# Performance work log

Measured on AMD Instinct MI355X. Metric: run time of the kernel, lower is better.

The kernel has to match this reference:

```python
import jax, jax.numpy as jnp
import numpy as np

E = 1024
H = 16
D = E // H
NUM_BUCKETS = 320
MAX_DISTANCE = 800


def _relative_positions_bucket(relative_positions):
    # relative_positions: int32 [T, S]
    num_buckets = NUM_BUCKETS // 2  # 160
    relative_buckets = (relative_positions > 0).astype(jnp.int32) * num_buckets
    rel = jnp.abs(relative_positions)
    max_exact = num_buckets // 2  # 80
    is_small = rel < max_exact
    rel_f = jnp.maximum(rel, 1).astype(jnp.float32)
    large = jnp.log(rel_f / max_exact) / np.log(MAX_DISTANCE / max_exact) * (num_buckets - max_exact)
    large = (max_exact + large).astype(jnp.int32)
    large = jnp.minimum(large, num_buckets - 1)
    relative_buckets = relative_buckets + jnp.where(is_small, rel, large)
    return relative_buckets


def setup_inputs() -> dict:
    key = jax.random.key(0)
    ks = jax.random.split(key, 12)
    B, T = 2, 2048
    s = 0.02
    return {
        "hidden_states": jax.random.normal(ks[0], (B, T, E), dtype=jnp.float32),
        "q_w": jax.random.normal(ks[1], (E, E), dtype=jnp.float32) * s,
        "q_b": jnp.zeros((E,), dtype=jnp.float32),
        "k_w": jax.random.normal(ks[2], (E, E), dtype=jnp.float32) * s,
        "k_b": jnp.zeros((E,), dtype=jnp.float32),
        "v_w": jax.random.normal(ks[3], (E, E), dtype=jnp.float32) * s,
        "v_b": jnp.zeros((E,), dtype=jnp.float32),
        "out_w": jax.random.normal(ks[4], (E, E), dtype=jnp.float32) * s,
        "out_b": jnp.zeros((E,), dtype=jnp.float32),
        "rel_embed": jax.random.normal(ks[5], (NUM_BUCKETS, H), dtype=jnp.float32) * s,
        "gru_const": jnp.ones((1, H, 1, 1), dtype=jnp.float32),
        "gru_w": jax.random.normal(ks[6], (8, D), dtype=jnp.float32) * s,
        "gru_b": jnp.zeros((8,), dtype=jnp.float32),
    }


def reference(hidden_states, q_w, q_b, k_w, k_b, v_w, v_b, out_w, out_b,
              rel_embed, gru_const, gru_w, gru_b):
    B, T, _ = hidden_states.shape
    scaling = D ** (-0.5)

    # --- relative position bias: [H, T, T] ---
    ctx = jnp.arange(T, dtype=jnp.int32)[:, None]
    mem = jnp.arange(T, dtype=jnp.int32)[None, :]
    buckets = _relative_positions_bucket(mem - ctx)          # [T, T]
    position_bias = rel_embed[buckets]                        # [T, T, H]
    position_bias = jnp.transpose(position_bias, (2, 0, 1))   # [H, T, T]

    # --- gate (gru_rel_pos): per (b, h, t) scalar ---
    gated = hidden_states.reshape(B, T, H, D).transpose(0, 2, 1, 3)  # [B,H,T,D]
    proj = jnp.einsum('bhtd,ed->bhte', gated, gru_w) + gru_b         # [B,H,T,8]
    proj = proj.reshape(B, H, T, 2, 4).sum(-1)                        # [B,H,T,2]
    gate = jax.nn.sigmoid(proj)
    gate_a = gate[..., 0:1]
    gate_b = gate[..., 1:2]
    gate_out = gate_a * (gate_b * gru_const - 1.0) + 2.0              # [B,H,T,1]
    gated_position_bias = gate_out * position_bias[None]              # [B,H,T,T]

    # --- attention (same math as F.multi_head_attention_forward eager path) ---
    q = (hidden_states @ q_w.T + q_b).reshape(B, T, H, D).transpose(0, 2, 1, 3) * scaling
    k = (hidden_states @ k_w.T + k_b).reshape(B, T, H, D).transpose(0, 2, 1, 3)
    v = (hidden_states @ v_w.T + v_b).reshape(B, T, H, D).transpose(0, 2, 1, 3)

    scores = jnp.einsum('bhtd,bhsd->bhts', q, k) + gated_position_bias
    attn = jax.nn.softmax(scores, axis=-1)
    ctx_out = jnp.einsum('bhts,bhsd->bhtd', attn, v)                  # [B,H,T,D]
    ctx_out = ctx_out.transpose(0, 2, 1, 3).reshape(B, T, E)
    return ctx_out @ out_w.T + out_b
```

## Files before the change

kernel.cpp:

```cpp
#include <hip/hip_runtime.h>
#include <hip/hip_bf16.h>
#include <math.h>

typedef __bf16 bf16;
typedef __bf16 bf16x4 __attribute__((ext_vector_type(4)));
typedef __bf16 bf16x8 __attribute__((ext_vector_type(8)));
typedef float  f32x4  __attribute__((ext_vector_type(4)));
typedef unsigned u32x2 __attribute__((ext_vector_type(2)));
typedef unsigned u32x4 __attribute__((ext_vector_type(4)));

#define T_SEQ 2048
#define E_DIM 1024
#define H_NUM 16
#define D_DIM 64
#define NDELTA 4095
#define LOG2E 1.4426950408889634f

__device__ __forceinline__ void gld16(const bf16* g, bf16* l) {
  __builtin_amdgcn_global_load_lds((__attribute__((address_space(1))) void*)(g),
                                   (__attribute__((address_space(3))) void*)(l), 16, 0, 0);
}

__device__ __forceinline__ void qswap(unsigned &a, unsigned &b) {
  u32x2 t  = __builtin_amdgcn_permlane32_swap(a, b, false, false);
  u32x2 t2 = __builtin_amdgcn_permlane16_swap(t[0], t[1], false, false);
  a = t2[0]; b = t2[1];
}

__global__ void cast_bf16_kernel(const float* __restrict__ src, bf16* __restrict__ dst, int n4) {
  int i = blockIdx.x * blockDim.x + threadIdx.x;
  if (i >= n4) return;
  const float4 v = reinterpret_cast<const float4*>(src)[i];
  bf16x4 o;
  o[0] = (bf16)v.x; o[1] = (bf16)v.y; o[2] = (bf16)v.z; o[3] = (bf16)v.w;
  reinterpret_cast<bf16x4*>(dst)[i] = o;
}

__global__ void cast_w_kernel(const float* __restrict__ q_w, const float* __restrict__ k_w,
                              const float* __restrict__ v_w, const float* __restrict__ o_w,
                              bf16* __restrict__ wcat, bf16* __restrict__ wob) {
  int i = blockIdx.x * 256 + threadIdx.x;
  int sel = blockIdx.y;
  const float* src = (sel == 0) ? q_w : (sel == 1) ? k_w : (sel == 2) ? v_w : o_w;
  bf16* dst = (sel < 3) ? (wcat + (size_t)sel * 1048576) : wob;
  const float4 v = reinterpret_cast<const float4*>(src)[i];
  bf16x4 o;
  o[0] = (bf16)v.x; o[1] = (bf16)v.y; o[2] = (bf16)v.z; o[3] = (bf16)v.w;
  reinterpret_cast<bf16x4*>(dst)[i] = o;
}

__global__ void pb_kernel(const float* __restrict__ rel_embed, float* __restrict__ pbt) {
  int dd = blockIdx.x * 64 + threadIdx.x;
  if (dd >= NDELTA) return;
  int delta = dd - (T_SEQ - 1);
  int bucket = (delta > 0) ? 160 : 0;
  int rel = abs(delta);
  int v;
  if (rel < 80) {
    v = rel;
  } else {
    float rf = (float)(rel < 1 ? 1 : rel);
    float lf = logf(rf / 80.0f) * (80.0f / 2.302585092994046f);
    int lg = 80 + (int)lf;
    v = lg < 159 ? lg : 159;
  }
  bucket += v;
#pragma unroll
  for (int h = 0; h < H_NUM; h++)
    pbt[h * NDELTA + dd] = rel_embed[bucket * H_NUM + h];
}

__global__ __launch_bounds__(256)
void gate_kernel(const float* __restrict__ hs, const float* __restrict__ gru_w,
                 const float* __restrict__ gru_b, const float* __restrict__ gconst,
                 float* __restrict__ gate)
{
  __shared__ float w[512];
  int tid = threadIdx.x;
  w[tid] = gru_w[tid];
  w[tid + 256] = gru_w[tid + 256];
  __syncthreads();
  int idx = blockIdx.x * 256 + tid;
  int h  = idx & 15;
  int bt = idx >> 4;
  const float* x = hs + (size_t)bt * E_DIM + h * D_DIM;
  float acc[8] = {0,0,0,0,0,0,0,0};
  for (int d = 0; d < 64; d += 4) {
    float4 xv = *(const float4*)&x[d];
#pragma unroll
    for (int e = 0; e < 8; e++) {
      acc[e] += xv.x * w[e*64+d] + xv.y * w[e*64+d+1]
              + xv.z * w[e*64+d+2] + xv.w * w[e*64+d+3];
    }
  }
  float p0 = acc[0]+acc[1]+acc[2]+acc[3] + gru_b[0]+gru_b[1]+gru_b[2]+gru_b[3];
  float p1 = acc[4]+acc[5]+acc[6]+acc[7] + gru_b[4]+gru_b[5]+gru_b[6]+gru_b[7];
  float ga = 1.0f / (1.0f + expf(-p0));
  float gb = 1.0f / (1.0f + expf(-p1));
  float g = (ga * (gb * gconst[h] - 1.0f) + 2.0f) * LOG2E;
  int bb = bt >> 11;
  int t  = bt & (T_SEQ - 1);
  gate[((size_t)(bb * H_NUM + h)) * T_SEQ + t] = g;
}

template<int MODE, int N_TOTAL>
__global__ __launch_bounds__(256)
void gemm2_kernel(const bf16* __restrict__ A, const bf16* __restrict__ W,
                  const float* __restrict__ b0, const float* __restrict__ b1,
                  const float* __restrict__ b2, float qalpha,
                  void* __restrict__ out0, void* __restrict__ out1, void* __restrict__ out2)
{
  __shared__ bf16 As[128 * 32];
  __shared__ bf16 Bs[128 * 32];
  const int tid  = threadIdx.x;
  const int lane = tid & 63;
  const int wave = tid >> 6;
  const int m0 = blockIdx.y * 128;
  const int n0 = blockIdx.x * 128;
  const int wm = (wave >> 1) * 64;
  const int wn = (wave & 1) * 64;
  const int qd = lane >> 4;
  const int lm = lane & 15;

  const int row4 = lane >> 2;
  const int col8 = (lane & 3) * 8;
  const bf16* gA0 = A + (size_t)(m0 + wave * 32 + row4) * 1024 + col8;
  const bf16* gA1 = gA0 + (size_t)16 * 1024;
  const bf16* gB0 = W + (size_t)(n0 + wave * 32 + row4) * 1024 + col8;
  const bf16* gB1 = gB0 + (size_t)16 * 1024;
  bf16* lA0 = As + (wave * 2 + 0) * 512;
  bf16* lA1 = As + (wave * 2 + 1) * 512;
  bf16* lB0 = Bs + (wave * 2 + 0) * 512;
  bf16* lB1 = Bs + (wave * 2 + 1) * 512;

  f32x4 acc[4][4] = {};

  for (int k0 = 0; k0 < 1024; k0 += 32) {
    gld16(gA0 + k0, lA0);
    gld16(gA1 + k0, lA1);
    gld16(gB0 + k0, lB0);
    gld16(gB1 + k0, lB1);
    __syncthreads();
    bf16x8 af[4], bfr[4];
#pragma unroll
    for (int i = 0; i < 4; i++) {
      af[i]  = *(const bf16x8*)&As[(wm + i * 16 + lm) * 32 + qd * 8];
      bfr[i] = *(const bf16x8*)&Bs[(wn + i * 16 + lm) * 32 + qd * 8];
    }
#pragma unroll
    for (int im = 0; im < 4; im++)
#pragma unroll
      for (int in = 0; in < 4; in++)
        acc[im][in] = __builtin_amdgcn_mfma_f32_16x16x32_bf16(af[im], bfr[in], acc[im][in], 0, 0, 0);
    __syncthreads();
  }

  const int seg = n0 >> 10;
  const float* bias = (MODE == 0) ? b0 : (seg == 0 ? b0 : (seg == 1 ? b1 : b2));
  const float alpha = (MODE == 1 && seg == 0) ? qalpha : 1.0f;

#pragma unroll
  for (int im = 0; im < 4; im++) {
#pragma unroll
    for (int in = 0; in < 4; in++) {
      const int n  = n0 + wn + in * 16 + lm;
      const int n1 = n & 1023;
      const float bv = bias[n1];
      const int mb = m0 + wm + im * 16 + qd * 4;
      if (MODE == 0) {
        float* o = (float*)out0;
#pragma unroll
        for (int r = 0; r < 4; r++)
          o[(size_t)(mb + r) * 1024 + n1] = acc[im][in][r] + bv;
      } else if (seg == 2) {
        const int bb = mb >> 11;
        const int t  = mb & 2047;
        bf16x4 pk;
#pragma unroll
        for (int r = 0; r < 4; r++) pk[r] = (bf16)(acc[im][in][r] + bv);
        *(bf16x4*)&((bf16*)out2)[((size_t)(bb * 1024 + n1)) * 2048 + t] = pk;
      } else {
        bf16* o = (bf16*)(seg == 0 ? out0 : out1);
#pragma unroll
        for (int r = 0; r < 4; r++)
          o[(size_t)(mb + r) * 1024 + n1] = (bf16)((acc[im][in][r] + bv) * alpha);
      }
    }
  }
}

#define LK 72
__global__ __launch_bounds__(256)
void attn3_kernel(const bf16* __restrict__ Qg, const bf16* __restrict__ Kg,
                  const bf16* __restrict__ Vtg, const float* __restrict__ gate,
                  const float* __restrict__ pbt, bf16* __restrict__ ctx)
{
  __shared__ bf16 Ks[2][64 * LK];
  __shared__ bf16 Vs[2][64 * LK];
  __shared__ float pbs[2176];

  const int t0 = blockIdx.x * 128;
  const int h  = blockIdx.y;
  const int b  = blockIdx.z;
  const int tid  = threadIdx.x;
  const int lane = tid & 63;
  const int wave = tid >> 6;
  const int qd = lane >> 4;
  const int lm = lane & 15;

  for (int i = tid; i < 2176; i += 256) {
    int idx = i - t0 + 1920;
    pbs[i] = (idx >= 0 && idx < NDELTA) ? pbt[h * NDELTA + idx] : 0.0f;
  }

  bf16x8 qf[2][2];
  float g[2];
#pragma unroll
  for (int nb = 0; nb < 2; nb++) {
    const int q = t0 + wave * 32 + nb * 16 + lm;
    const bf16* qrow = Qg + (size_t)(b * T_SEQ + q) * E_DIM + h * D_DIM;
    qf[nb][0] = *(const bf16x8*)(qrow + qd * 8);
    qf[nb][1] = *(const bf16x8*)(qrow + 32 + qd * 8);
    g[nb] = gate[((size_t)(b * H_NUM + h)) * T_SEQ + q];
  }

  const int srow = tid >> 2;
  const int scol = (tid & 3) * 16;
  const bf16* kgp = Kg  + ((size_t)(b * T_SEQ) + srow) * E_DIM + h * D_DIM + scol;
  const bf16* vgp = Vtg + ((size_t)(b * 1024) + h * D_DIM + srow) * T_SEQ + scol;

  {
    bf16x8 a0 = *(const bf16x8*)kgp;
    bf16x8 a1 = *(const bf16x8*)(kgp + 8);
    bf16x8 c0 = *(const bf16x8*)vgp;
    bf16x8 c1 = *(const bf16x8*)(vgp + 8);
    *(bf16x8*)&Ks[0][srow * LK + scol]     = a0;
    *(bf16x8*)&Ks[0][srow * LK + scol + 8] = a1;
    *(bf16x8*)&Vs[0][srow * LK + scol]     = c0;
    *(bf16x8*)&Vs[0][srow * LK + scol + 8] = c1;
  }
  __syncthreads();

  f32x4 o[4][2] = {};
  float li[2] = {0.0f, 0.0f};

  for (int it = 0; it < T_SEQ / 64; it++) {
    const int s0 = it * 64;
    const int buf = it & 1;
    const bool more = (it + 1 < T_SEQ / 64);
    bf16x8 nk0, nk1, nv0, nv1;
    if (more) {
      const bf16* kn = kgp + (size_t)(s0 + 64) * E_DIM;
      const bf16* vn = vgp + (s0 + 64);
      nk0 = *(const bf16x8*)kn; nk1 = *(const bf16x8*)(kn + 8);
      nv0 = *(const bf16x8*)vn; nv1 = *(const bf16x8*)(vn + 8);
    }

    bf16x8 kf[4][2];
#pragma unroll
    for (int mb = 0; mb < 4; mb++) {
      kf[mb][0] = *(const bf16x8*)&Ks[buf][(16 * mb + lm) * LK + qd * 8];
      kf[mb][1] = *(const bf16x8*)&Ks[buf][(16 * mb + lm) * LK + 32 + qd * 8];
    }

    bf16x8 pf[2][2];
#pragma unroll
    for (int nb = 0; nb < 2; nb++) {
      f32x4 sc[4];
#pragma unroll
      for (int mb = 0; mb < 4; mb++) {
        f32x4 t = {};
        t = __builtin_amdgcn_mfma_f32_16x16x32_bf16(kf[mb][0], qf[nb][0], t, 0, 0, 0);
        t = __builtin_amdgcn_mfma_f32_16x16x32_bf16(kf[mb][1], qf[nb][1], t, 0, 0, 0);
        sc[mb] = t;
      }
      const int ib = s0 + 4 * qd + 127 - (wave * 32 + nb * 16 + lm);
      float rs = 0.0f;
      unsigned wlo[4], whi[4];
#pragma unroll
      for (int mb = 0; mb < 4; mb++) {
        bf16x4 pk;
#pragma unroll
        for (int r = 0; r < 4; r++) {
          float p = __builtin_amdgcn_exp2f(sc[mb][r] + g[nb] * pbs[ib + 16 * mb + r]);
          rs += p;
          pk[r] = (bf16)p;
        }
        u32x2 pw = __builtin_bit_cast(u32x2, pk);
        wlo[mb] = pw[0]; whi[mb] = pw[1];
      }
      li[nb] += rs;
      unsigned a0 = wlo[0], b0v = wlo[1], a1 = whi[0], b1v = whi[1];
      qswap(a0, b0v);
      qswap(a1, b1v);
      u32x4 h0; h0[0] = a0; h0[1] = a1; h0[2] = b0v; h0[3] = b1v;
      pf[nb][0] = __builtin_bit_cast(bf16x8, h0);
      unsigned c0 = wlo[2], d0v = wlo[3], c1 = whi[2], d1v = whi[3];
      qswap(c0, d0v);
      qswap(c1, d1v);
      u32x4 h1; h1[0] = c0; h1[1] = c1; h1[2] = d0v; h1[3] = d1v;
      pf[nb][1] = __builtin_bit_cast(bf16x8, h1);
    }

#pragma unroll
    for (int db = 0; db < 4; db++) {
      bf16x8 vf0 = *(const bf16x8*)&Vs[buf][(16 * db + lm) * LK + qd * 8];
      bf16x8 vf1 = *(const bf16x8*)&Vs[buf][(16 * db + lm) * LK + 32 + qd * 8];
#pragma unroll
      for (int nb = 0; nb < 2; nb++) {
        o[db][nb] = __builtin_amdgcn_mfma_f32_16x16x32_bf16(vf0, pf[nb][0], o[db][nb], 0, 0, 0);
        o[db][nb] = __builtin_amdgcn_mfma_f32_16x16x32_bf16(vf1, pf[nb][1], o[db][nb], 0, 0, 0);
      }
    }
    if (more) {
      *(bf16x8*)&Ks[buf ^ 1][srow * LK + scol]     = nk0;
      *(bf16x8*)&Ks[buf ^ 1][srow * LK + scol + 8] = nk1;
      *(bf16x8*)&Vs[buf ^ 1][srow * LK + scol]     = nv0;
      *(bf16x8*)&Vs[buf ^ 1][srow * LK + scol + 8] = nv1;
    }
    __syncthreads();
  }

#pragma unroll
  for (int nb = 0; nb < 2; nb++) {
    li[nb] += __shfl_xor(li[nb], 16);
    li[nb] += __shfl_xor(li[nb], 32);
  }
#pragma unroll
  for (int nb = 0; nb < 2; nb++) {
    const float inv = 1.0f / li[nb];
    const int q = t0 + wave * 32 + nb * 16 + lm;
    bf16* obase = ctx + (size_t)(b * T_SEQ + q) * E_DIM + h * D_DIM + 4 * qd;
#pragma unroll
    for (int db = 0; db < 4; db++) {
      bf16x4 ov;
      ov[0] = (bf16)(o[db][nb][0] * inv); ov[1] = (bf16)(o[db][nb][1] * inv);
      ov[2] = (bf16)(o[db][nb][2] * inv); ov[3] = (bf16)(o[db][nb][3] * inv);
      *(bf16x4*)&obase[16 * db] = ov;
    }
  }
}

extern "C" void kernel_launch(void* const* d_in, const int* in_sizes, int n_in,
                              void* d_out, int out_size, void* d_ws, size_t ws_size,
                              hipStream_t stream)
{
  const float* hs     = (const float*)d_in[0];
  const float* q_w    = (const float*)d_in[1];
  const float* q_b    = (const float*)d_in[2];
  const float* k_w    = (const float*)d_in[3];
  const float* k_b    = (const float*)d_in[4];
  const float* v_w    = (const float*)d_in[5];
  const float* v_b    = (const float*)d_in[6];
  const float* out_w  = (const float*)d_in[7];
  const float* out_b  = (const float*)d_in[8];
  const float* rel    = (const float*)d_in[9];
  const float* gconst = (const float*)d_in[10];
  const float* gru_w  = (const float*)d_in[11];
  const float* gru_b  = (const float*)d_in[12];

  char* p = (char*)d_ws;
  bf16* hsb  = (bf16*)p; p += (size_t)4096 * 1024 * 2;
  bf16* wcat = (bf16*)p; p += (size_t)3072 * 1024 * 2;
  bf16* wob  = (bf16*)p; p += (size_t)1024 * 1024 * 2;
  bf16* Qb   = (bf16*)p; p += (size_t)4096 * 1024 * 2;
  bf16* Kb   = (bf16*)p; p += (size_t)4096 * 1024 * 2;
  bf16* Vtb  = (bf16*)p; p += (size_t)2048 * 2048 * 2;
  bf16* ctxb = (bf16*)p; p += (size_t)4096 * 1024 * 2;
  float* gatep = (float*)p; p += (size_t)2 * H_NUM * T_SEQ * 4;
  float* pbt   = (float*)p; p += (size_t)H_NUM * NDELTA * 4;

  cast_bf16_kernel<<<4096, 256, 0, stream>>>(hs, hsb, 1048576);
  cast_w_kernel<<<dim3(1024, 4), 256, 0, stream>>>(q_w, k_w, v_w, out_w, wcat, wob);
  pb_kernel<<<64, 64, 0, stream>>>(rel, pbt);
  gate_kernel<<<256, 256, 0, stream>>>(hs, gru_w, gru_b, gconst, gatep);

  const float qalpha = 0.125f * LOG2E;
  gemm2_kernel<1, 3072><<<dim3(24, 32), 256, 0, stream>>>(
      hsb, wcat, q_b, k_b, v_b, qalpha, Qb, Kb, Vtb);

  attn3_kernel<<<dim3(T_SEQ / 128, H_NUM, 2), 256, 0, stream>>>(Qb, Kb, Vtb, gatep, pbt, ctxb);

  gemm2_kernel<0, 1024><<<dim3(8, 32), 256, 0, stream>>>(
      ctxb, wob, out_b, nullptr, nullptr, 1.0f, d_out, nullptr, nullptr);
}
```

Baseline: 223.5 us.

## Load K/V tiles directly into LDS with XOR swizzle and MFMA priority hints

The attention kernel's K and V tile loads now go straight from global memory into LDS through global_load_lds. This replaces the register-staged loads and the LDS stores at the end of each iteration. The padded LDS layout is dropped in favour of an XOR-swizzled column layout to avoid bank conflicts. s_setprio is also raised around the MFMA sections. The intent is to cut VGPR pressure and instruction overhead in the loop, and to overlap the prefetch better. The risk is that the async LDS writes rely on the existing barrier for correctness.

```diff
diff --git a/kernel.cpp b/kernel.cpp
--- a/kernel.cpp
+++ b/kernel.cpp
@@ -189,14 +189,13 @@
   }
 }
 
-#define LK 72
 __global__ __launch_bounds__(256)
 void attn3_kernel(const bf16* __restrict__ Qg, const bf16* __restrict__ Kg,
                   const bf16* __restrict__ Vtg, const float* __restrict__ gate,
                   const float* __restrict__ pbt, bf16* __restrict__ ctx)
 {
-  __shared__ bf16 Ks[2][64 * LK];
-  __shared__ bf16 Vs[2][64 * LK];
+  __shared__ bf16 Ks[2][64 * 64];
+  __shared__ bf16 Vs[2][64 * 64];
   __shared__ float pbs[2176];
 
   const int t0 = blockIdx.x * 128;
@@ -224,56 +223,57 @@
     g[nb] = gate[((size_t)(b * H_NUM + h)) * T_SEQ + q];
   }
 
-  const int srow = tid >> 2;
-  const int scol = (tid & 3) * 16;
-  const bf16* kgp = Kg  + ((size_t)(b * T_SEQ) + srow) * E_DIM + h * D_DIM + scol;
-  const bf16* vgp = Vtg + ((size_t)(b * 1024) + h * D_DIM + srow) * T_SEQ + scol;
-
-  {
-    bf16x8 a0 = *(const bf16x8*)kgp;
-    bf16x8 a1 = *(const bf16x8*)(kgp + 8);
-    bf16x8 c0 = *(const bf16x8*)vgp;
-    bf16x8 c1 = *(const bf16x8*)(vgp + 8);
-    *(bf16x8*)&Ks[0][srow * LK + scol]     = a0;
-    *(bf16x8*)&Ks[0][srow * LK + scol + 8] = a1;
-    *(bf16x8*)&Vs[0][srow * LK + scol]     = c0;
-    *(bf16x8*)&Vs[0][srow * LK + scol + 8] = c1;
-  }
+  const int sr = lane >> 3;
+  const int sc = ((lane & 7) ^ sr) * 8;
+  const bf16* kg0 = Kg  + ((size_t)(b * T_SEQ) + wave * 16 + sr) * E_DIM + h * D_DIM + sc;
+  const bf16* kg1 = kg0 + (size_t)8 * E_DIM;
+  const bf16* vg0 = Vtg + ((size_t)(b * 1024) + h * D_DIM + wave * 16 + sr) * T_SEQ + sc;
+  const bf16* vg1 = vg0 + (size_t)8 * T_SEQ;
+  const int l0 = (wave * 16 + 0) * 64;
+  const int l1 = (wave * 16 + 8) * 64;
+
+  gld16(kg0, &Ks[0][l0]);
+  gld16(kg1, &Ks[0][l1]);
+  gld16(vg0, &Vs[0][l0]);
+  gld16(vg1, &Vs[0][l1]);
   __syncthreads();
 
   f32x4 o[4][2] = {};
   float li[2] = {0.0f, 0.0f};
+  const int xs = lm & 7;
 
   for (int it = 0; it < T_SEQ / 64; it++) {
     const int s0 = it * 64;
     const int buf = it & 1;
     const bool more = (it + 1 < T_SEQ / 64);
-    bf16x8 nk0, nk1, nv0, nv1;
     if (more) {
-      const bf16* kn = kgp + (size_t)(s0 + 64) * E_DIM;
-      const bf16* vn = vgp + (s0 + 64);
-      nk0 = *(const bf16x8*)kn; nk1 = *(const bf16x8*)(kn + 8);
-      nv0 = *(const bf16x8*)vn; nv1 = *(const bf16x8*)(vn + 8);
+      const size_t ko = (size_t)(s0 + 64) * E_DIM;
+      gld16(kg0 + ko, &Ks[buf ^ 1][l0]);
+      gld16(kg1 + ko, &Ks[buf ^ 1][l1]);
+      gld16(vg0 + (s0 + 64), &Vs[buf ^ 1][l0]);
+      gld16(vg1 + (s0 + 64), &Vs[buf ^ 1][l1]);
     }
 
     bf16x8 kf[4][2];
 #pragma unroll
     for (int mb = 0; mb < 4; mb++) {
-      kf[mb][0] = *(const bf16x8*)&Ks[buf][(16 * mb + lm) * LK + qd * 8];
-      kf[mb][1] = *(const bf16x8*)&Ks[buf][(16 * mb + lm) * LK + 32 + qd * 8];
+      kf[mb][0] = *(const bf16x8*)&Ks[buf][(16 * mb + lm) * 64 + ((qd ^ xs) * 8)];
+      kf[mb][1] = *(const bf16x8*)&Ks[buf][(16 * mb + lm) * 64 + (((qd + 4) ^ xs) * 8)];
     }
 
     bf16x8 pf[2][2];
 #pragma unroll
     for (int nb = 0; nb < 2; nb++) {
-      f32x4 sc[4];
+      f32x4 sc4[4];
+      __builtin_amdgcn_s_setprio(1);
 #pragma unroll
       for (int mb = 0; mb < 4; mb++) {
         f32x4 t = {};
         t = __builtin_amdgcn_mfma_f32_16x16x32_bf16(kf[mb][0], qf[nb][0], t, 0, 0, 0);
         t = __builtin_amdgcn_mfma_f32_16x16x32_bf16(kf[mb][1], qf[nb][1], t, 0, 0, 0);
-        sc[mb] = t;
+        sc4[mb] = t;
       }
+      __builtin_amdgcn_s_setprio(0);
       const int ib = s0 + 4 * qd + 127 - (wave * 32 + nb * 16 + lm);
       float rs = 0.0f;
       unsigned wlo[4], whi[4];
@@ -282,7 +282,7 @@
         bf16x4 pk;
 #pragma unroll
         for (int r = 0; r < 4; r++) {
-          float p = __builtin_amdgcn_exp2f(sc[mb][r] + g[nb] * pbs[ib + 16 * mb + r]);
+          float p = __builtin_amdgcn_exp2f(sc4[mb][r] + g[nb] * pbs[ib + 16 * mb + r]);
           rs += p;
           pk[r] = (bf16)p;
         }
@@ -302,22 +302,18 @@
       pf[nb][1] = __builtin_bit_cast(bf16x8, h1);
     }
 
+    __builtin_amdgcn_s_setprio(1);
 #pragma unroll
     for (int db = 0; db < 4; db++) {
-      bf16x8 vf0 = *(const bf16x8*)&Vs[buf][(16 * db + lm) * LK + qd * 8];
-      bf16x8 vf1 = *(const bf16x8*)&Vs[buf][(16 * db + lm) * LK + 32 + qd * 8];
+      bf16x8 vf0 = *(const bf16x8*)&Vs[buf][(16 * db + lm) * 64 + ((qd ^ xs) * 8)];
+      bf16x8 vf1 = *(const bf16x8*)&Vs[buf][(16 * db + lm) * 64 + (((qd + 4) ^ xs) * 8)];
 #pragma unroll
       for (int nb = 0; nb < 2; nb++) {
         o[db][nb] = __builtin_amdgcn_mfma_f32_16x16x32_bf16(vf0, pf[nb][0], o[db][nb], 0, 0, 0);
         o[db][nb] = __builtin_amdgcn_mfma_f32_16x16x32_bf16(vf1, pf[nb][1], o[db][nb], 0, 0, 0);
       }
     }
-    if (more) {
-      *(bf16x8*)&Ks[buf ^ 1][srow * LK + scol]     = nk0;
-      *(bf16x8*)&Ks[buf ^ 1][srow * LK + scol + 8] = nk1;
-      *(bf16x8*)&Vs[buf ^ 1][srow * LK + scol]     = nv0;
-      *(bf16x8*)&Vs[buf ^ 1][srow * LK + scol + 8] = nv1;
-    }
+    __builtin_amdgcn_s_setprio(0);
     __syncthreads();
   }
 
```

New measurement: 228.4 us. +2.2%, slower.
